# Kernel optimization log

Hardware: AMD Instinct MI355X
Metric: run time of the kernel (lower is better)

The kernel has to match this reference:

```python
import jax, jax.numpy as jnp
import numpy as np

EPS = 1e-8  # matches torch CosineSimilarity eps and the +1e-08 in mean_attentive


def setup_inputs() -> dict:
    key = jax.random.key(0)
    k1, k2, k3 = jax.random.split(key, 3)
    B, L1, L2, D, P = 16, 512, 512, 1024, 10
    sent1 = jax.random.normal(k1, (B, L1, D), dtype=jnp.float32)
    sent2 = jax.random.normal(k2, (B, L2, D), dtype=jnp.float32)
    kernel = jax.random.normal(k3, (P, 1), dtype=jnp.float32)
    return {"sent1": sent1, "sent2": sent2, "kernel": kernel}


def reference(sent1, sent2, kernel):
    # Cross-sentence cosine similarity matrix: [B, L1, L2]
    dot = jnp.einsum('bld,bmd->blm', sent1, sent2)
    n1 = jnp.linalg.norm(sent1, axis=-1)  # [B, L1]
    n2 = jnp.linalg.norm(sent2, axis=-1)  # [B, L2]
    cos_matrix = dot / jnp.maximum(n1[:, :, None] * n2[:, None, :], EPS)

    # Mean attentive vectors over sent2: [B, L1, D]
    weighted_sum = jnp.einsum('blm,bmd->bld', cos_matrix, sent2)
    sum_cos = jnp.sum(cos_matrix, axis=-1, keepdims=True) + 1e-8
    mean_attentive = weighted_sum / sum_cos

    # Multi-perspective scaling by kernel [P, 1] -> [B, L1, P, D]
    v1 = sent1[:, :, None, :] * kernel
    v2 = mean_attentive[:, :, None, :] * kernel

    # Cosine similarity over D: [B, L1, P]
    dot2 = jnp.sum(v1 * v2, axis=-1)
    denom = jnp.maximum(jnp.linalg.norm(v1, axis=-1) * jnp.linalg.norm(v2, axis=-1), EPS)
    return dot2 / denom
```

## Files before the change

kernel.cpp:

```cpp
#include <hip/hip_runtime.h>
#include <hip/hip_bf16.h>
#include <math.h>

#define Bn 16
#define Ln 512
#define Dn 1024
#define Pn 10

typedef short bf16x8 __attribute__((ext_vector_type(8)));
typedef float f32x4 __attribute__((ext_vector_type(4)));

__device__ __forceinline__ short2 bf16split(float x) {
    __hip_bfloat16 h = __float2bfloat16(x);
    float hf = __bfloat162float(h);
    __hip_bfloat16 l = __float2bfloat16(x - hf);
    short2 r;
    __builtin_memcpy(&r.x, &h, 2);
    __builtin_memcpy(&r.y, &l, 2);
    return r;
}

__global__ __launch_bounds__(256) void norms_kernel(const float* __restrict__ s1,
                                                    const float* __restrict__ s2,
                                                    float* __restrict__ nrm) {
    const int wave = threadIdx.x >> 6;
    const int lane = threadIdx.x & 63;
    const int row  = blockIdx.x * 4 + wave;
    const float* src = (row < Bn * Ln) ? (s1 + (size_t)row * Dn)
                                       : (s2 + (size_t)(row - Bn * Ln) * Dn);
    const float4* p4 = (const float4*)src;
    float acc = 0.f;
#pragma unroll
    for (int i = 0; i < 4; ++i) {
        float4 v = p4[lane + i * 64];
        acc = fmaf(v.x, v.x, acc);
        acc = fmaf(v.y, v.y, acc);
        acc = fmaf(v.z, v.z, acc);
        acc = fmaf(v.w, v.w, acc);
    }
#pragma unroll
    for (int m = 32; m; m >>= 1) acc += __shfl_xor(acc, m, 64);
    if (lane == 0) nrm[row] = sqrtf(acc);
}

__global__ __launch_bounds__(256) void prep_s2_kernel(const float* __restrict__ s2,
                                                      short* __restrict__ s2nh,
                                                      short* __restrict__ s2nl,
                                                      short* __restrict__ s2th,
                                                      short* __restrict__ s2tl) {
    __shared__ float tile[64][65];
    const int tid = threadIdx.x;
    const int tb  = blockIdx.x;
    const int b   = tb >> 7;
    const int rem = tb & 127;
    const int l2c = (rem >> 4) * 64;
    const int dc  = (rem & 15) * 64;

#pragma unroll
    for (int i = 0; i < 4; ++i) {
        int r  = (tid >> 4) + 16 * i;
        int c4 = (tid & 15) * 4;
        float4 v = *(const float4*)(s2 + ((size_t)b * Ln + l2c + r) * Dn + dc + c4);
        tile[r][c4 + 0] = v.x;
        tile[r][c4 + 1] = v.y;
        tile[r][c4 + 2] = v.z;
        tile[r][c4 + 3] = v.w;
        short2 p0 = bf16split(v.x), p1 = bf16split(v.y),
               p2 = bf16split(v.z), p3 = bf16split(v.w);
        short4 h; h.x = p0.x; h.y = p1.x; h.z = p2.x; h.w = p3.x;
        short4 l; l.x = p0.y; l.y = p1.y; l.z = p2.y; l.w = p3.y;
        size_t noff = ((size_t)b * Ln + l2c + r) * Dn + dc + c4;
        *(short4*)(s2nh + noff) = h;
        *(short4*)(s2nl + noff) = l;
    }
    __syncthreads();
#pragma unroll
    for (int i = 0; i < 2; ++i) {
        int dr  = (tid >> 3) + 32 * i;
        int l2o = (tid & 7) * 8;
        bf16x8 hv, lv;
#pragma unroll
        for (int j = 0; j < 8; ++j) {
            short2 p = bf16split(tile[l2o + j][dr]);
            hv[j] = p.x;
            lv[j] = p.y;
        }
        size_t off = ((size_t)b * Dn + dc + dr) * Ln + l2c + l2o;
        *(bf16x8*)(s2th + off) = hv;
        *(bf16x8*)(s2tl + off) = lv;
    }
}

__global__ __launch_bounds__(1024, 4) void mfma_fused_kernel(
        const float* __restrict__ s1,
        const float* __restrict__ kern, const float* __restrict__ nrm,
        const short* __restrict__ s2nh, const short* __restrict__ s2nl,
        const short* __restrict__ s2th, const short* __restrict__ s2tl,
        float* __restrict__ out) {
    __shared__ float Sr[32][516];
    __shared__ short Ah[2][32][136];
    __shared__ short Al[2][32][136];
    __shared__ float n2c[Ln];
    __shared__ float n1c[32];
    __shared__ float scl[32];
    __shared__ float red[32][32];
    __shared__ float redS[32][16];
    __shared__ float redD[32][16];
    __shared__ float kc_[16];

    const int tid  = threadIdx.x;
    const int w    = tid >> 6;
    const int lane = tid & 63;
    const int lr   = lane & 15;
    const int lg   = lane >> 4;

    const int wg = ((blockIdx.x & 7) << 5) | (blockIdx.x >> 3);
    const int b  = wg >> 4;
    const int R0 = (wg & 15) * 32;

    const float* s1b = s1 + ((size_t)b * Ln + R0) * Dn;
    const size_t s2row0  = (size_t)b * Ln;
    const size_t s2trow0 = (size_t)b * Dn;

    if (tid < 32) n1c[tid] = nrm[b * Ln + R0 + tid];
    if (tid < Ln) n2c[tid] = nrm[Bn * Ln + b * Ln + tid];
    if (tid < Pn) kc_[tid] = kern[tid];

    auto stageA = [&](int buf, int kb) {
        int r = tid >> 5, k = (tid & 31) * 4;
        float4 v = *(const float4*)(s1b + (size_t)r * Dn + kb + k);
        short2 p0 = bf16split(v.x), p1 = bf16split(v.y),
               p2 = bf16split(v.z), p3 = bf16split(v.w);
        short4 h; h.x = p0.x; h.y = p1.x; h.z = p2.x; h.w = p3.x;
        short4 l; l.x = p0.y; l.y = p1.y; l.z = p2.y; l.w = p3.y;
        *(short4*)&Ah[buf][r][k] = h;
        *(short4*)&Al[buf][r][k] = l;
    };

    f32x4 accA[2][2];
#pragma unroll
    for (int m = 0; m < 2; ++m)
#pragma unroll
        for (int t = 0; t < 2; ++t) accA[m][t] = (f32x4){0.f, 0.f, 0.f, 0.f};

    stageA(0, 0);
    __syncthreads();

    for (int kb = 0; kb < Dn; kb += 128) {
        int cur = (kb >> 7) & 1;
        if (kb + 128 < Dn) stageA(cur ^ 1, kb + 128);
#pragma unroll
        for (int ks = 0; ks < 128; ks += 32) {
            bf16x8 ah[2], al[2];
#pragma unroll
            for (int m = 0; m < 2; ++m) {
                ah[m] = *(const bf16x8*)&Ah[cur][m * 16 + lr][ks + lg * 8];
                al[m] = *(const bf16x8*)&Al[cur][m * 16 + lr][ks + lg * 8];
            }
#pragma unroll
            for (int t = 0; t < 2; ++t) {
                int l2 = (w * 2 + t) * 16 + lr;
                size_t off = (s2row0 + l2) * Dn + kb + ks + lg * 8;
                bf16x8 bh = *(const bf16x8*)(s2nh + off);
                bf16x8 bl = *(const bf16x8*)(s2nl + off);
#pragma unroll
                for (int m = 0; m < 2; ++m) {
                    accA[m][t] = __builtin_amdgcn_mfma_f32_16x16x32_bf16(ah[m], bh, accA[m][t], 0, 0, 0);
                    accA[m][t] = __builtin_amdgcn_mfma_f32_16x16x32_bf16(ah[m], bl, accA[m][t], 0, 0, 0);
                    accA[m][t] = __builtin_amdgcn_mfma_f32_16x16x32_bf16(al[m], bh, accA[m][t], 0, 0, 0);
                }
            }
        }
        __syncthreads();
    }
#pragma unroll
    for (int m = 0; m < 2; ++m)
#pragma unroll
        for (int t = 0; t < 2; ++t)
#pragma unroll
            for (int reg = 0; reg < 4; ++reg)
                Sr[m * 16 + lg * 4 + reg][(w * 2 + t) * 16 + lr] = accA[m][t][reg];
    __syncthreads();

    {
        int r = tid >> 5, part = tid & 31;
        float n1v = n1c[r];
        float s = 0.f;
#pragma unroll 8
        for (int j = 0; j < 16; ++j) {
            int l2 = part + 32 * j;
            float d = Sr[r][l2];
            float c = d / fmaxf(n1v * n2c[l2], 1e-8f);
            Sr[r][l2] = c;
            s += c;
        }
        red[r][part] = s;
    }
    __syncthreads();
    if (tid < 32) {
        float s = 0.f;
#pragma unroll
        for (int j = 0; j < 32; ++j) s += red[tid][j];
        scl[tid] = s + 1e-8f;
    }
    __syncthreads();

    f32x4 accB[2][4];
#pragma unroll
    for (int m = 0; m < 2; ++m)
#pragma unroll
        for (int t = 0; t < 4; ++t) accB[m][t] = (f32x4){0.f, 0.f, 0.f, 0.f};

    for (int kc = 0; kc < Ln; kc += 32) {
        bf16x8 ah[2], al[2];
#pragma unroll
        for (int m = 0; m < 2; ++m) {
            const float* ap = &Sr[m * 16 + lr][kc + lg * 8];
            float4 v0 = *(const float4*)ap;
            float4 v1 = *(const float4*)(ap + 4);
            float f[8] = {v0.x, v0.y, v0.z, v0.w, v1.x, v1.y, v1.z, v1.w};
#pragma unroll
            for (int j = 0; j < 8; ++j) {
                short2 p = bf16split(f[j]);
                ah[m][j] = p.x;
                al[m][j] = p.y;
            }
        }
#pragma unroll
        for (int t = 0; t < 4; ++t) {
            int d = (w * 4 + t) * 16 + lr;
            size_t off = (s2trow0 + d) * Ln + kc + lg * 8;
            bf16x8 bh = *(const bf16x8*)(s2th + off);
            bf16x8 bl = *(const bf16x8*)(s2tl + off);
#pragma unroll
            for (int m = 0; m < 2; ++m) {
                accB[m][t] = __builtin_amdgcn_mfma_f32_16x16x32_bf16(ah[m], bh, accB[m][t], 0, 0, 0);
                accB[m][t] = __builtin_amdgcn_mfma_f32_16x16x32_bf16(ah[m], bl, accB[m][t], 0, 0, 0);
                accB[m][t] = __builtin_amdgcn_mfma_f32_16x16x32_bf16(al[m], bh, accB[m][t], 0, 0, 0);
            }
        }
    }

    float ss[2][4], sd[2][4];
#pragma unroll
    for (int m = 0; m < 2; ++m)
#pragma unroll
        for (int reg = 0; reg < 4; ++reg) { ss[m][reg] = 0.f; sd[m][reg] = 0.f; }

#pragma unroll
    for (int m = 0; m < 2; ++m)
#pragma unroll
        for (int t = 0; t < 4; ++t) {
            int d = (w * 4 + t) * 16 + lr;
#pragma unroll
            for (int reg = 0; reg < 4; ++reg) {
                int row = m * 16 + lg * 4 + reg;
                float wv = accB[m][t][reg];
                ss[m][reg] = fmaf(wv, wv, ss[m][reg]);
                float x = s1b[(size_t)row * Dn + d];
                sd[m][reg] = fmaf(x, wv, sd[m][reg]);
            }
        }
#pragma unroll
    for (int m = 0; m < 2; ++m)
#pragma unroll
        for (int reg = 0; reg < 4; ++reg) {
#pragma unroll
            for (int msk = 8; msk; msk >>= 1) {
                ss[m][reg] += __shfl_xor(ss[m][reg], msk, 64);
                sd[m][reg] += __shfl_xor(sd[m][reg], msk, 64);
            }
        }
    if (lr == 0) {
#pragma unroll
        for (int m = 0; m < 2; ++m)
#pragma unroll
            for (int reg = 0; reg < 4; ++reg) {
                redS[m * 16 + lg * 4 + reg][w] = ss[m][reg];
                redD[m * 16 + lg * 4 + reg][w] = sd[m][reg];
            }
    }
    __syncthreads();

    if (tid < 32 * Pn) {
        int r = tid / Pn, p = tid % Pn;
        float ssT = 0.f, sdT = 0.f;
#pragma unroll
        for (int j = 0; j < 16; ++j) { ssT += redS[r][j]; sdT += redD[r][j]; }
        float n1v = n1c[r];
        float scv = scl[r];
        float kp  = kc_[p];
        float kp2 = kp * kp;
        float wsn = sqrtf(ssT);
        float dot2  = kp2 * sdT / scv;
        float denom = fmaxf(kp2 * n1v * wsn / fabsf(scv), 1e-8f);
        out[(size_t)(b * Ln + R0 + r) * Pn + p] = dot2 / denom;
    }
}

#define Mr 16
#define LD2 516

__global__ __launch_bounds__(256, 2) void fused_kernel(const float* __restrict__ s1,
                                                       const float* __restrict__ s2,
                                                       const float* __restrict__ kern,
                                                       const float* __restrict__ nrm,
                                                       float* __restrict__ out) {
    __shared__ float Sr[Mr][LD2];
    __shared__ float s2t[16][LD2];
    __shared__ float ab[16][16];
    __shared__ float n2c[Ln];
    __shared__ float n1c[Mr];
    __shared__ float scl[Mr];
    __shared__ float red[Mr][16];
    __shared__ float redS[Mr][2];
    __shared__ float redD[Mr][2];
    __shared__ float kc_[16];

    const int tid  = threadIdx.x;
    const int w    = tid >> 6;
    const int lane = tid & 63;
    const int rg   = w & 1;
    const int cg   = w >> 1;

    const int wg = ((blockIdx.x & 7) << 6) | (blockIdx.x >> 3);
    const int b  = wg >> 5;
    const int R0 = (wg & 31) * Mr;

    const float* s1b = s1 + ((size_t)b * Ln + R0) * Dn;
    const float* s2g = s2 + (size_t)b * Ln * Dn;

    if (tid < Mr) n1c[tid] = nrm[b * Ln + R0 + tid];
    n2c[tid]       = nrm[Bn * Ln + b * Ln + tid];
    n2c[tid + 256] = nrm[Bn * Ln + b * Ln + tid + 256];
    if (tid < Pn) kc_[tid] = kern[tid];

    float accA[8][4];
#pragma unroll
    for (int e = 0; e < 8; ++e)
#pragma unroll
        for (int c = 0; c < 4; ++c) accA[e][c] = 0.f;

    for (int kc = 0; kc < Dn; kc += 16) {
        __syncthreads();
        {
            int r = tid >> 4, k = tid & 15;
            ab[k][r] = s1b[(size_t)r * Dn + kc + k];
        }
        {
            int p = tid >> 2, j = tid & 3;
#pragma unroll
            for (int ri = 0; ri < 8; ++ri) {
                int l2 = ri * 64 + p;
                float4 v = *(const float4*)(s2g + (size_t)l2 * Dn + kc + 4 * j);
                s2t[4 * j + 0][l2] = v.x;
                s2t[4 * j + 1][l2] = v.y;
                s2t[4 * j + 2][l2] = v.z;
                s2t[4 * j + 3][l2] = v.w;
            }
        }
        __syncthreads();
#pragma unroll
        for (int k = 0; k < 16; ++k) {
            float4 a0 = *(const float4*)&ab[k][rg * 8];
            float4 a1 = *(const float4*)&ab[k][rg * 8 + 4];
            float4 bv = *(const float4*)&s2t[k][cg * 256 + 4 * lane];
            float aa[8] = {a0.x, a0.y, a0.z, a0.w, a1.x, a1.y, a1.z, a1.w};
            float bb[4] = {bv.x, bv.y, bv.z, bv.w};
#pragma unroll
            for (int e = 0; e < 8; ++e)
#pragma unroll
                for (int c = 0; c < 4; ++c)
                    accA[e][c] = fmaf(aa[e], bb[c], accA[e][c]);
        }
    }
#pragma unroll
    for (int e = 0; e < 8; ++e)
        *(float4*)&Sr[rg * 8 + e][cg * 256 + 4 * lane] =
            make_float4(accA[e][0], accA[e][1], accA[e][2], accA[e][3]);
    __syncthreads();

    {
        int r = tid >> 4, part = tid & 15;
        float n1v = n1c[r];
        float s = 0.f;
#pragma unroll 8
        for (int j = 0; j < 32; ++j) {
            int l2 = part + 16 * j;
            float d = Sr[r][l2];
            float c = d / fmaxf(n1v * n2c[l2], 1e-8f);
            Sr[r][l2] = c;
            s += c;
        }
        red[r][part] = s;
    }
    __syncthreads();
    if (tid < Mr) {
        float s = 0.f;
#pragma unroll
        for (int j = 0; j < 16; ++j) s += red[tid][j];
        scl[tid] = s + 1e-8f;
    }

    float ss[8] = {0.f, 0.f, 0.f, 0.f, 0.f, 0.f, 0.f, 0.f};
    float sd[8] = {0.f, 0.f, 0.f, 0.f, 0.f, 0.f, 0.f, 0.f};

    for (int dh = 0; dh < Dn; dh += 512) {
        float accB[8][4];
#pragma unroll
        for (int e = 0; e < 8; ++e)
#pragma unroll
            for (int c = 0; c < 4; ++c) accB[e][c] = 0.f;

        for (int l2c = 0; l2c < Ln; l2c += 16) {
            __syncthreads();
            {
                int l2 = tid >> 4, r = tid & 15;
                ab[l2][r] = Sr[r][l2c + l2];
            }
            {
                int l2 = tid >> 4, q = tid & 15;
                const float* srcrow = s2g + (size_t)(l2c + l2) * Dn + dh;
#pragma unroll
                for (int j = 0; j < 8; ++j)
                    *(float4*)&s2t[l2][q * 4 + j * 64] =
                        *(const float4*)(srcrow + q * 4 + j * 64);
            }
            __syncthreads();
#pragma unroll
            for (int k = 0; k < 16; ++k) {
                float4 a0 = *(const float4*)&ab[k][rg * 8];
                float4 a1 = *(const float4*)&ab[k][rg * 8 + 4];
                float4 bv = *(const float4*)&s2t[k][cg * 256 + 4 * lane];
                float aa[8] = {a0.x, a0.y, a0.z, a0.w, a1.x, a1.y, a1.z, a1.w};
                float bb[4] = {bv.x, bv.y, bv.z, bv.w};
#pragma unroll
                for (int e = 0; e < 8; ++e)
#pragma unroll
                    for (int c = 0; c < 4; ++c)
                        accB[e][c] = fmaf(aa[e], bb[c], accB[e][c]);
            }
        }
#pragma unroll
        for (int e = 0; e < 8; ++e) {
            const float* s1row = s1b + (size_t)(rg * 8 + e) * Dn + dh + cg * 256 + 4 * lane;
            float4 x = *(const float4*)s1row;
            float xx[4] = {x.x, x.y, x.z, x.w};
#pragma unroll
            for (int c = 0; c < 4; ++c) {
                float wv = accB[e][c];
                ss[e] = fmaf(wv, wv, ss[e]);
                sd[e] = fmaf(xx[c], wv, sd[e]);
            }
        }
    }

#pragma unroll
    for (int e = 0; e < 8; ++e) {
#pragma unroll
        for (int m = 32; m; m >>= 1) {
            ss[e] += __shfl_xor(ss[e], m, 64);
            sd[e] += __shfl_xor(sd[e], m, 64);
        }
    }
    if (lane == 0) {
#pragma unroll
        for (int e = 0; e < 8; ++e) {
            redS[rg * 8 + e][cg] = ss[e];
            redD[rg * 8 + e][cg] = sd[e];
        }
    }
    __syncthreads();

    if (tid < Mr * Pn) {
        int r = tid / Pn, p = tid % Pn;
        float ssT = redS[r][0] + redS[r][1];
        float sdT = redD[r][0] + redD[r][1];
        float n1v = n1c[r];
        float scv = scl[r];
        float kp  = kc_[p];
        float kp2 = kp * kp;
        float wsn = sqrtf(ssT);
        float dot2  = kp2 * sdT / scv;
        float denom = fmaxf(kp2 * n1v * wsn / fabsf(scv), 1e-8f);
        out[(size_t)(b * Ln + R0 + r) * Pn + p] = dot2 / denom;
    }
}

extern "C" void kernel_launch(void* const* d_in, const int* in_sizes, int n_in,
                              void* d_out, int out_size, void* d_ws, size_t ws_size,
                              hipStream_t stream) {
    const float* s1   = (const float*)d_in[0];
    const float* s2   = (const float*)d_in[1];
    const float* kern = (const float*)d_in[2];
    float* out = (float*)d_out;

    char* w = (char*)d_ws;
    float* nrm = (float*)w;
    const size_t SZ1 = (size_t)Bn * Ln * Dn * sizeof(short);
    short* s2nh = (short*)(w + 65536);
    short* s2nl = (short*)(w + 65536 + SZ1);
    short* s2th = (short*)(w + 65536 + 2 * SZ1);
    short* s2tl = (short*)(w + 65536 + 3 * SZ1);
    const size_t NEED = 65536 + 4 * SZ1;

    hipLaunchKernelGGL(norms_kernel, dim3((Bn * Ln * 2) / 4), dim3(256), 0, stream,
                       s1, s2, nrm);

    if (ws_size >= NEED) {
        hipLaunchKernelGGL(prep_s2_kernel, dim3(Bn * 8 * 16), dim3(256), 0, stream,
                           s2, s2nh, s2nl, s2th, s2tl);
        hipLaunchKernelGGL(mfma_fused_kernel, dim3(Bn * (Ln / 32)), dim3(1024), 0, stream,
                           s1, kern, nrm, s2nh, s2nl, s2th, s2tl, out);
    } else {
        hipLaunchKernelGGL(fused_kernel, dim3(Bn * (Ln / Mr)), dim3(256), 0, stream,
                           s1, s2, kern, nrm, out);
    }
}
```

Measured before the change: 230.5 us.

## Split fused MFMA kernel into cosine, fold and epilogue kernels with larger tiles

Replaces the single fused MFMA kernel with three kernels. The first computes the cosine matrix in 64x256 tiles and writes it to workspace as a bf16 hi/lo split, plus per-half row sums. The second multiplies that matrix by transposed sent2 over 64 rows by 512 D columns, reducing ss/sd partials. A small epilogue then combines the partials into the outputs. The aim is larger tiles and more reuse of the s2 operands per block; in exchange the cosine matrix now makes a round trip through global memory, there are two extra launches, and the path needs more workspace. The fallback fp32 fused kernel is removed, so with too little workspace nothing is launched.

```diff
diff --git a/kernel.cpp b/kernel.cpp
--- a/kernel.cpp
+++ b/kernel.cpp
@@ -89,6 +89,267 @@
         *(bf16x8*)(s2th + off) = hv;
         *(bf16x8*)(s2tl + off) = lv;
     }
+}
+
+__global__ __launch_bounds__(1024) void cos_kernel(
+        const float* __restrict__ s1, const float* __restrict__ nrm,
+        const short* __restrict__ s2nh, const short* __restrict__ s2nl,
+        short* __restrict__ cosH, short* __restrict__ cosL,
+        float* __restrict__ sumP) {
+    __shared__ float Sr[64][260];
+    __shared__ short Ah[2][64][72];
+    __shared__ short Al[2][64][72];
+    __shared__ float n1c[64];
+    __shared__ float n2c[256];
+    __shared__ float red[64][16];
+
+    const int tid  = threadIdx.x;
+    const int w    = tid >> 6;
+    const int lane = tid & 63;
+    const int lr   = lane & 15;
+    const int lg   = lane >> 4;
+    const int p    = w >> 3;
+    const int c    = w & 7;
+
+    const int wg   = ((blockIdx.x & 7) << 5) | (blockIdx.x >> 3);
+    const int m8   = wg & 7;
+    const int bh   = wg >> 3;
+    const int half = bh & 1;
+    const int b    = bh >> 1;
+    const int R0   = m8 * 64;
+
+    const float* s1b = s1 + ((size_t)b * Ln + R0) * Dn;
+    const size_t s2row0 = (size_t)b * Ln + half * 256;
+
+    if (tid < 64)  n1c[tid] = nrm[b * Ln + R0 + tid];
+    if (tid < 256) n2c[tid] = nrm[Bn * Ln + b * Ln + half * 256 + tid];
+
+    auto stageA = [&](int buf, int kb) {
+        int r = tid >> 4, k4 = (tid & 15) * 4;
+        float4 v = *(const float4*)(s1b + (size_t)r * Dn + kb + k4);
+        short2 p0 = bf16split(v.x), p1 = bf16split(v.y),
+               p2 = bf16split(v.z), p3 = bf16split(v.w);
+        short4 h; h.x = p0.x; h.y = p1.x; h.z = p2.x; h.w = p3.x;
+        short4 l; l.x = p0.y; l.y = p1.y; l.z = p2.y; l.w = p3.y;
+        *(short4*)&Ah[buf][r][k4] = h;
+        *(short4*)&Al[buf][r][k4] = l;
+    };
+
+    f32x4 acc[2][2];
+#pragma unroll
+    for (int pm = 0; pm < 2; ++pm)
+#pragma unroll
+        for (int tt = 0; tt < 2; ++tt) acc[pm][tt] = (f32x4){0.f, 0.f, 0.f, 0.f};
+
+    stageA(0, 0);
+    __syncthreads();
+
+    for (int kb = 0; kb < Dn; kb += 64) {
+        int cur = (kb >> 6) & 1;
+        if (kb + 64 < Dn) stageA(cur ^ 1, kb + 64);
+#pragma unroll
+        for (int ks = 0; ks < 64; ks += 32) {
+            bf16x8 ah[2], al[2];
+#pragma unroll
+            for (int pm = 0; pm < 2; ++pm) {
+                int row = p * 32 + pm * 16 + lr;
+                ah[pm] = *(const bf16x8*)&Ah[cur][row][ks + lg * 8];
+                al[pm] = *(const bf16x8*)&Al[cur][row][ks + lg * 8];
+            }
+#pragma unroll
+            for (int tt = 0; tt < 2; ++tt) {
+                int l2 = (2 * c + tt) * 16 + lr;
+                size_t off = (s2row0 + l2) * Dn + kb + ks + lg * 8;
+                bf16x8 bhv = *(const bf16x8*)(s2nh + off);
+                bf16x8 blv = *(const bf16x8*)(s2nl + off);
+#pragma unroll
+                for (int pm = 0; pm < 2; ++pm) {
+                    acc[pm][tt] = __builtin_amdgcn_mfma_f32_16x16x32_bf16(ah[pm], bhv, acc[pm][tt], 0, 0, 0);
+                    acc[pm][tt] = __builtin_amdgcn_mfma_f32_16x16x32_bf16(ah[pm], blv, acc[pm][tt], 0, 0, 0);
+                    acc[pm][tt] = __builtin_amdgcn_mfma_f32_16x16x32_bf16(al[pm], bhv, acc[pm][tt], 0, 0, 0);
+                }
+            }
+        }
+        __syncthreads();
+    }
+#pragma unroll
+    for (int pm = 0; pm < 2; ++pm)
+#pragma unroll
+        for (int tt = 0; tt < 2; ++tt)
+#pragma unroll
+            for (int reg = 0; reg < 4; ++reg)
+                Sr[p * 32 + pm * 16 + lg * 4 + reg][(2 * c + tt) * 16 + lr] = acc[pm][tt][reg];
+    __syncthreads();
+
+    {
+        int r = tid >> 4, part = tid & 15;
+        float n1v = n1c[r];
+        short* cH = cosH + ((size_t)b * Ln + R0 + r) * Ln + half * 256;
+        short* cL = cosL + ((size_t)b * Ln + R0 + r) * Ln + half * 256;
+        float s = 0.f;
+#pragma unroll 4
+        for (int j = 0; j < 16; ++j) {
+            int l2 = part + 16 * j;
+            float d = Sr[r][l2];
+            float cv = d / fmaxf(n1v * n2c[l2], 1e-8f);
+            short2 sp = bf16split(cv);
+            cH[l2] = sp.x;
+            cL[l2] = sp.y;
+            s += cv;
+        }
+        red[r][part] = s;
+    }
+    __syncthreads();
+    if (tid < 64) {
+        float s = 0.f;
+#pragma unroll
+        for (int j = 0; j < 16; ++j) s += red[tid][j];
+        sumP[((size_t)b * Ln + R0 + tid) * 2 + half] = s;
+    }
+}
+
+__global__ __launch_bounds__(1024) void fold_kernel(
+        const float* __restrict__ s1,
+        const short* __restrict__ s2th, const short* __restrict__ s2tl,
+        const short* __restrict__ cosH, const short* __restrict__ cosL,
+        float* __restrict__ ssP, float* __restrict__ sdP) {
+    __shared__ short ChH[2][64][72];
+    __shared__ short ChL[2][64][72];
+    __shared__ float redS[64][8];
+    __shared__ float redD[64][8];
+
+    const int tid  = threadIdx.x;
+    const int w    = tid >> 6;
+    const int lane = tid & 63;
+    const int lr   = lane & 15;
+    const int lg   = lane >> 4;
+    const int p    = w >> 3;
+    const int c    = w & 7;
+
+    const int wg   = ((blockIdx.x & 7) << 5) | (blockIdx.x >> 3);
+    const int m8   = wg & 7;
+    const int bh   = wg >> 3;
+    const int dh   = bh & 1;
+    const int b    = bh >> 1;
+    const int R0   = m8 * 64;
+
+    const float* s1b = s1 + ((size_t)b * Ln + R0) * Dn;
+    const size_t cosrow0 = (size_t)b * Ln + R0;
+    const size_t s2trow0 = (size_t)b * Dn + dh * 512;
+
+    auto stageC = [&](int buf, int kc) {
+        int r = tid >> 4, q4 = (tid & 15) * 4;
+        *(short4*)&ChH[buf][r][q4] = *(const short4*)(cosH + (cosrow0 + r) * Ln + kc + q4);
+        *(short4*)&ChL[buf][r][q4] = *(const short4*)(cosL + (cosrow0 + r) * Ln + kc + q4);
+    };
+
+    f32x4 acc[2][4];
+#pragma unroll
+    for (int pm = 0; pm < 2; ++pm)
+#pragma unroll
+        for (int j = 0; j < 4; ++j) acc[pm][j] = (f32x4){0.f, 0.f, 0.f, 0.f};
+
+    stageC(0, 0);
+    __syncthreads();
+
+    for (int kc = 0; kc < Ln; kc += 64) {
+        int cur = (kc >> 6) & 1;
+        if (kc + 64 < Ln) stageC(cur ^ 1, kc + 64);
+#pragma unroll
+        for (int ks = 0; ks < 64; ks += 32) {
+            bf16x8 ah[2], al[2];
+#pragma unroll
+            for (int pm = 0; pm < 2; ++pm) {
+                int row = p * 32 + pm * 16 + lr;
+                ah[pm] = *(const bf16x8*)&ChH[cur][row][ks + lg * 8];
+                al[pm] = *(const bf16x8*)&ChL[cur][row][ks + lg * 8];
+            }
+#pragma unroll
+            for (int j = 0; j < 4; ++j) {
+                int d = (c * 4 + j) * 16 + lr;
+                size_t off = (s2trow0 + d) * Ln + kc + ks + lg * 8;
+                bf16x8 bhv = *(const bf16x8*)(s2th + off);
+                bf16x8 blv = *(const bf16x8*)(s2tl + off);
+#pragma unroll
+                for (int pm = 0; pm < 2; ++pm) {
+                    acc[pm][j] = __builtin_amdgcn_mfma_f32_16x16x32_bf16(ah[pm], bhv, acc[pm][j], 0, 0, 0);
+                    acc[pm][j] = __builtin_amdgcn_mfma_f32_16x16x32_bf16(ah[pm], blv, acc[pm][j], 0, 0, 0);
+                    acc[pm][j] = __builtin_amdgcn_mfma_f32_16x16x32_bf16(al[pm], bhv, acc[pm][j], 0, 0, 0);
+                }
+            }
+        }
+        __syncthreads();
+    }
+
+    float ss[2][4], sd[2][4];
+#pragma unroll
+    for (int pm = 0; pm < 2; ++pm)
+#pragma unroll
+        for (int reg = 0; reg < 4; ++reg) { ss[pm][reg] = 0.f; sd[pm][reg] = 0.f; }
+
+#pragma unroll
+    for (int pm = 0; pm < 2; ++pm)
+#pragma unroll
+        for (int j = 0; j < 4; ++j) {
+            int d = dh * 512 + (c * 4 + j) * 16 + lr;
+#pragma unroll
+            for (int reg = 0; reg < 4; ++reg) {
+                int row = p * 32 + pm * 16 + lg * 4 + reg;
+                float wv = acc[pm][j][reg];
+                ss[pm][reg] = fmaf(wv, wv, ss[pm][reg]);
+                float x = s1b[(size_t)row * Dn + d];
+                sd[pm][reg] = fmaf(x, wv, sd[pm][reg]);
+            }
+        }
+#pragma unroll
+    for (int pm = 0; pm < 2; ++pm)
+#pragma unroll
+        for (int reg = 0; reg < 4; ++reg) {
+#pragma unroll
+            for (int msk = 8; msk; msk >>= 1) {
+                ss[pm][reg] += __shfl_xor(ss[pm][reg], msk, 64);
+                sd[pm][reg] += __shfl_xor(sd[pm][reg], msk, 64);
+            }
+        }
+    if (lr == 0) {
+#pragma unroll
+        for (int pm = 0; pm < 2; ++pm)
+#pragma unroll
+            for (int reg = 0; reg < 4; ++reg) {
+                int row = p * 32 + pm * 16 + lg * 4 + reg;
+                redS[row][c] = ss[pm][reg];
+                redD[row][c] = sd[pm][reg];
+            }
+    }
+    __syncthreads();
+
+    if (tid < 64) {
+        float sS = 0.f, sD = 0.f;
+#pragma unroll
+        for (int j = 0; j < 8; ++j) { sS += redS[tid][j]; sD += redD[tid][j]; }
+        size_t o = ((size_t)b * Ln + R0 + tid) * 2 + dh;
+        ssP[o] = sS;
+        sdP[o] = sD;
+    }
+}
+
+__global__ __launch_bounds__(256) void epi_kernel(
+        const float* __restrict__ nrm, const float* __restrict__ kern,
+        const float* __restrict__ sumP, const float* __restrict__ ssP,
+        const float* __restrict__ sdP, float* __restrict__ out) {
+    int idx = blockIdx.x * 256 + threadIdx.x;
+    int r = idx >> 4, pp = idx & 15;
+    if (pp >= Pn) return;
+    float ssT = ssP[r * 2] + ssP[r * 2 + 1];
+    float sdT = sdP[r * 2] + sdP[r * 2 + 1];
+    float scv = sumP[r * 2] + sumP[r * 2 + 1] + 1e-8f;
+    float n1v = nrm[r];
+    float kp  = kern[pp];
+    float kp2 = kp * kp;
+    float wsn = sqrtf(ssT);
+    float dot2  = kp2 * sdT / scv;
+    float denom = fmaxf(kp2 * n1v * wsn / fabsf(scv), 1e-8f);
+    out[(size_t)r * Pn + pp] = dot2 / denom;
 }
 
 __global__ __launch_bounds__(1024, 4) void mfma_fused_kernel(
@@ -190,9 +451,9 @@
         for (int j = 0; j < 16; ++j) {
             int l2 = part + 32 * j;
             float d = Sr[r][l2];
-            float c = d / fmaxf(n1v * n2c[l2], 1e-8f);
-            Sr[r][l2] = c;
-            s += c;
+            float cv = d / fmaxf(n1v * n2c[l2], 1e-8f);
+            Sr[r][l2] = cv;
+            s += cv;
         }
         red[r][part] = s;
     }
@@ -221,9 +482,9 @@
             float f[8] = {v0.x, v0.y, v0.z, v0.w, v1.x, v1.y, v1.z, v1.w};
 #pragma unroll
             for (int j = 0; j < 8; ++j) {
-                short2 p = bf16split(f[j]);
-                ah[m][j] = p.x;
-                al[m][j] = p.y;
+                short2 pz = bf16split(f[j]);
+                ah[m][j] = pz.x;
+                al[m][j] = pz.y;
             }
         }
 #pragma unroll
@@ -283,207 +544,18 @@
     __syncthreads();
 
     if (tid < 32 * Pn) {
-        int r = tid / Pn, p = tid % Pn;
+        int r = tid / Pn, pq = tid % Pn;
         float ssT = 0.f, sdT = 0.f;
 #pragma unroll
         for (int j = 0; j < 16; ++j) { ssT += redS[r][j]; sdT += redD[r][j]; }
         float n1v = n1c[r];
         float scv = scl[r];
-        float kp  = kc_[p];
+        float kp  = kc_[pq];
         float kp2 = kp * kp;
         float wsn = sqrtf(ssT);
         float dot2  = kp2 * sdT / scv;
         float denom = fmaxf(kp2 * n1v * wsn / fabsf(scv), 1e-8f);
-        out[(size_t)(b * Ln + R0 + r) * Pn + p] = dot2 / denom;
-    }
-}
-
-#define Mr 16
-#define LD2 516
-
-__global__ __launch_bounds__(256, 2) void fused_kernel(const float* __restrict__ s1,
-                                                       const float* __restrict__ s2,
-                                                       const float* __restrict__ kern,
-                                                       const float* __restrict__ nrm,
-                                                       float* __restrict__ out) {
-    __shared__ float Sr[Mr][LD2];
-    __shared__ float s2t[16][LD2];
-    __shared__ float ab[16][16];
-    __shared__ float n2c[Ln];
-    __shared__ float n1c[Mr];
-    __shared__ float scl[Mr];
-    __shared__ float red[Mr][16];
-    __shared__ float redS[Mr][2];
-    __shared__ float redD[Mr][2];
-    __shared__ float kc_[16];
-
-    const int tid  = threadIdx.x;
-    const int w    = tid >> 6;
-    const int lane = tid & 63;
-    const int rg   = w & 1;
-    const int cg   = w >> 1;
-
-    const int wg = ((blockIdx.x & 7) << 6) | (blockIdx.x >> 3);
-    const int b  = wg >> 5;
-    const int R0 = (wg & 31) * Mr;
-
-    const float* s1b = s1 + ((size_t)b * Ln + R0) * Dn;
-    const float* s2g = s2 + (size_t)b * Ln * Dn;
-
-    if (tid < Mr) n1c[tid] = nrm[b * Ln + R0 + tid];
-    n2c[tid]       = nrm[Bn * Ln + b * Ln + tid];
-    n2c[tid + 256] = nrm[Bn * Ln + b * Ln + tid + 256];
-    if (tid < Pn) kc_[tid] = kern[tid];
-
-    float accA[8][4];
-#pragma unroll
-    for (int e = 0; e < 8; ++e)
-#pragma unroll
-        for (int c = 0; c < 4; ++c) accA[e][c] = 0.f;
-
-    for (int kc = 0; kc < Dn; kc += 16) {
-        __syncthreads();
-        {
-            int r = tid >> 4, k = tid & 15;
-            ab[k][r] = s1b[(size_t)r * Dn + kc + k];
-        }
-        {
-            int p = tid >> 2, j = tid & 3;
-#pragma unroll
-            for (int ri = 0; ri < 8; ++ri) {
-                int l2 = ri * 64 + p;
-                float4 v = *(const float4*)(s2g + (size_t)l2 * Dn + kc + 4 * j);
-                s2t[4 * j + 0][l2] = v.x;
-                s2t[4 * j + 1][l2] = v.y;
-                s2t[4 * j + 2][l2] = v.z;
-                s2t[4 * j + 3][l2] = v.w;
-            }
-        }
-        __syncthreads();
-#pragma unroll
-        for (int k = 0; k < 16; ++k) {
-            float4 a0 = *(const float4*)&ab[k][rg * 8];
-            float4 a1 = *(const float4*)&ab[k][rg * 8 + 4];
-            float4 bv = *(const float4*)&s2t[k][cg * 256 + 4 * lane];
-            float aa[8] = {a0.x, a0.y, a0.z, a0.w, a1.x, a1.y, a1.z, a1.w};
-            float bb[4] = {bv.x, bv.y, bv.z, bv.w};
-#pragma unroll
-            for (int e = 0; e < 8; ++e)
-#pragma unroll
-                for (int c = 0; c < 4; ++c)
-                    accA[e][c] = fmaf(aa[e], bb[c], accA[e][c]);
-        }
-    }
-#pragma unroll
-    for (int e = 0; e < 8; ++e)
-        *(float4*)&Sr[rg * 8 + e][cg * 256 + 4 * lane] =
-            make_float4(accA[e][0], accA[e][1], accA[e][2], accA[e][3]);
-    __syncthreads();
-
-    {
-        int r = tid >> 4, part = tid & 15;
-        float n1v = n1c[r];
-        float s = 0.f;
-#pragma unroll 8
-        for (int j = 0; j < 32; ++j) {
-            int l2 = part + 16 * j;
-            float d = Sr[r][l2];
-            float c = d / fmaxf(n1v * n2c[l2], 1e-8f);
-            Sr[r][l2] = c;
-            s += c;
-        }
-        red[r][part] = s;
-    }
-    __syncthreads();
-    if (tid < Mr) {
-        float s = 0.f;
-#pragma unroll
-        for (int j = 0; j < 16; ++j) s += red[tid][j];
-        scl[tid] = s + 1e-8f;
-    }
-
-    float ss[8] = {0.f, 0.f, 0.f, 0.f, 0.f, 0.f, 0.f, 0.f};
-    float sd[8] = {0.f, 0.f, 0.f, 0.f, 0.f, 0.f, 0.f, 0.f};
-
-    for (int dh = 0; dh < Dn; dh += 512) {
-        float accB[8][4];
-#pragma unroll
-        for (int e = 0; e < 8; ++e)
-#pragma unroll
-            for (int c = 0; c < 4; ++c) accB[e][c] = 0.f;
-
-        for (int l2c = 0; l2c < Ln; l2c += 16) {
-            __syncthreads();
-            {
-                int l2 = tid >> 4, r = tid & 15;
-                ab[l2][r] = Sr[r][l2c + l2];
-            }
-            {
-                int l2 = tid >> 4, q = tid & 15;
-                const float* srcrow = s2g + (size_t)(l2c + l2) * Dn + dh;
-#pragma unroll
-                for (int j = 0; j < 8; ++j)
-                    *(float4*)&s2t[l2][q * 4 + j * 64] =
-                        *(const float4*)(srcrow + q * 4 + j * 64);
-            }
-            __syncthreads();
-#pragma unroll
-            for (int k = 0; k < 16; ++k) {
-                float4 a0 = *(const float4*)&ab[k][rg * 8];
-                float4 a1 = *(const float4*)&ab[k][rg * 8 + 4];
-                float4 bv = *(const float4*)&s2t[k][cg * 256 + 4 * lane];
-                float aa[8] = {a0.x, a0.y, a0.z, a0.w, a1.x, a1.y, a1.z, a1.w};
-                float bb[4] = {bv.x, bv.y, bv.z, bv.w};
-#pragma unroll
-                for (int e = 0; e < 8; ++e)
-#pragma unroll
-                    for (int c = 0; c < 4; ++c)
-                        accB[e][c] = fmaf(aa[e], bb[c], accB[e][c]);
-            }
-        }
-#pragma unroll
-        for (int e = 0; e < 8; ++e) {
-            const float* s1row = s1b + (size_t)(rg * 8 + e) * Dn + dh + cg * 256 + 4 * lane;
-            float4 x = *(const float4*)s1row;
-            float xx[4] = {x.x, x.y, x.z, x.w};
-#pragma unroll
-            for (int c = 0; c < 4; ++c) {
-                float wv = accB[e][c];
-                ss[e] = fmaf(wv, wv, ss[e]);
-                sd[e] = fmaf(xx[c], wv, sd[e]);
-            }
-        }
-    }
-
-#pragma unroll
-    for (int e = 0; e < 8; ++e) {
-#pragma unroll
-        for (int m = 32; m; m >>= 1) {
-            ss[e] += __shfl_xor(ss[e], m, 64);
-            sd[e] += __shfl_xor(sd[e], m, 64);
-        }
-    }
-    if (lane == 0) {
-#pragma unroll
-        for (int e = 0; e < 8; ++e) {
-            redS[rg * 8 + e][cg] = ss[e];
-            redD[rg * 8 + e][cg] = sd[e];
-        }
-    }
-    __syncthreads();
-
-    if (tid < Mr * Pn) {
-        int r = tid / Pn, p = tid % Pn;
-        float ssT = redS[r][0] + redS[r][1];
-        float sdT = redD[r][0] + redD[r][1];
-        float n1v = n1c[r];
-        float scv = scl[r];
-        float kp  = kc_[p];
-        float kp2 = kp * kp;
-        float wsn = sqrtf(ssT);
-        float dot2  = kp2 * sdT / scv;
-        float denom = fmaxf(kp2 * n1v * wsn / fabsf(scv), 1e-8f);
-        out[(size_t)(b * Ln + R0 + r) * Pn + p] = dot2 / denom;
+        out[(size_t)(b * Ln + R0 + r) * Pn + pq] = dot2 / denom;
     }
 }
 
@@ -498,22 +570,36 @@
     char* w = (char*)d_ws;
     float* nrm = (float*)w;
     const size_t SZ1 = (size_t)Bn * Ln * Dn * sizeof(short);
+    const size_t SZC = (size_t)Bn * Ln * Ln * sizeof(short);
+    const size_t SZP = (size_t)Bn * Ln * 2 * sizeof(float);
     short* s2nh = (short*)(w + 65536);
     short* s2nl = (short*)(w + 65536 + SZ1);
     short* s2th = (short*)(w + 65536 + 2 * SZ1);
     short* s2tl = (short*)(w + 65536 + 3 * SZ1);
-    const size_t NEED = 65536 + 4 * SZ1;
+    short* cosH = (short*)(w + 65536 + 4 * SZ1);
+    short* cosL = (short*)(w + 65536 + 4 * SZ1 + SZC);
+    float* sumP = (float*)(w + 65536 + 4 * SZ1 + 2 * SZC);
+    float* ssP  = (float*)(w + 65536 + 4 * SZ1 + 2 * SZC + SZP);
+    float* sdP  = (float*)(w + 65536 + 4 * SZ1 + 2 * SZC + 2 * SZP);
+    const size_t NEED1 = 65536 + 4 * SZ1;
+    const size_t NEED2 = 65536 + 4 * SZ1 + 2 * SZC + 3 * SZP;
 
     hipLaunchKernelGGL(norms_kernel, dim3((Bn * Ln * 2) / 4), dim3(256), 0, stream,
                        s1, s2, nrm);
 
-    if (ws_size >= NEED) {
+    if (ws_size >= NEED2) {
+        hipLaunchKernelGGL(prep_s2_kernel, dim3(Bn * 8 * 16), dim3(256), 0, stream,
+                           s2, s2nh, s2nl, s2th, s2tl);
+        hipLaunchKernelGGL(cos_kernel, dim3(256), dim3(1024), 0, stream,
+                           s1, nrm, s2nh, s2nl, cosH, cosL, sumP);
+        hipLaunchKernelGGL(fold_kernel, dim3(256), dim3(1024), 0, stream,
+                           s1, s2th, s2tl, cosH, cosL, ssP, sdP);
+        hipLaunchKernelGGL(epi_kernel, dim3(Bn * Ln * 16 / 256), dim3(256), 0, stream,
+                           nrm, kern, sumP, ssP, sdP, out);
+    } else if (ws_size >= NEED1) {
         hipLaunchKernelGGL(prep_s2_kernel, dim3(Bn * 8 * 16), dim3(256), 0, stream,
                            s2, s2nh, s2nl, s2th, s2tl);
         hipLaunchKernelGGL(mfma_fused_kernel, dim3(Bn * (Ln / 32)), dim3(1024), 0, stream,
                            s1, kern, nrm, s2nh, s2nl, s2th, s2tl, out);
-    } else {
-        hipLaunchKernelGGL(fused_kernel, dim3(Bn * (Ln / Mr)), dim3(256), 0, stream,
-                           s1, s2, kern, nrm, out);
-    }
-}
+    }
+}
```

After: 254.7 us. +10.5%, slower.
